# Performance work log

Measured on AMD Instinct MI355X. Metric: run time of the kernel, lower is better.

The kernel has to match this reference:

```python
import jax, jax.numpy as jnp
import numpy as np

N, T, E, E2 = 10000, 32, 320000, 160000
D, H = 128, 128
SLOPE = 0.01  # LeakyReLU negative slope (args.relu)


def _lstm_dir(x, mask, Wih, Whh, b, reverse):
    # x: [N,T,D], mask: [N,T] int; returns final hidden [N,H] honoring per-seq lengths
    xs = jnp.swapaxes(x, 0, 1)                                 # [T,N,D]
    ms = jnp.swapaxes(mask, 0, 1)[..., None].astype(x.dtype)   # [T,N,1]
    Hh = Whh.shape[1]
    h0 = jnp.zeros((x.shape[0], Hh), x.dtype)

    def step(carry, tm):
        h, c = carry
        xt, mt = tm
        g = xt @ Wih.T + h @ Whh.T + b                         # [N,4H], torch gate order i,f,g,o
        i, f, gg, o = jnp.split(g, 4, axis=-1)
        i, f, o = jax.nn.sigmoid(i), jax.nn.sigmoid(f), jax.nn.sigmoid(o)
        c_new = f * c + i * jnp.tanh(gg)
        h_new = o * jnp.tanh(c_new)
        h = mt * h_new + (1.0 - mt) * h
        c = mt * c_new + (1.0 - mt) * c
        return (h, c), None

    (h, _), _ = jax.lax.scan(step, (h0, h0), (xs, ms), reverse=reverse)
    return h


def _sage(h, src, dst, Wself, Wneigh, b):
    # DGL SAGEConv, mean aggregator: h@W_self + mean_neigh(h)@W_neigh + b
    n = h.shape[0]
    msum = jax.ops.segment_sum(h[src], dst, num_segments=n)
    deg = jax.ops.segment_sum(jnp.ones((src.shape[0],), h.dtype), dst, num_segments=n)
    neigh = msum / jnp.maximum(deg, 1.0)[:, None]
    return h @ Wself + neigh @ Wneigh + b


def setup_inputs():
    key = jax.random.key(0)
    ks = jax.random.split(key, 40)
    f = lambda i, shape: jax.random.normal(ks[i], shape, jnp.float32) * 0.05
    return dict(
        inputs_s=jax.random.randint(ks[0], (N, T), 0, 128, jnp.int32),
        inputs_sm=jnp.ones((N, T), jnp.int32),
        inputs_c=jax.random.randint(ks[1], (N,), 0, 101, jnp.int32),
        inputs_co=jax.random.randint(ks[2], (N,), 0, 92, jnp.int32),
        inputs_sl=jax.random.randint(ks[3], (N,), 0, 6, jnp.int32),
        inputs_ip=jax.random.normal(ks[4], (N, 32), jnp.float32),
        blk_src=jax.random.randint(ks[5], (E,), 0, N, jnp.int32),
        blk_dst=jax.random.randint(ks[6], (E,), 0, N, jnp.int32),
        e_src=jax.random.randint(ks[7], (E2,), 0, N, jnp.int32),
        e_dst=jax.random.randint(ks[8], (E2,), 0, N, jnp.int32),
        emb_url=f(9, (128, D)), emb_cat=f(10, (101, D)), emb_cou=f(11, (92, D)), emb_sl_t=f(12, (6, D)),
        Wih_f=f(13, (4 * D, D)), Whh_f=f(14, (4 * D, D)), b_f=f(15, (4 * D,)),
        Wih_b=f(16, (4 * D, D)), Whh_b=f(17, (4 * D, D)), b_b=f(18, (4 * D,)),
        fc_lstm_W=f(19, (2 * D, D)), fc_lstm_b=f(20, (D,)),
        attnlin_W=f(21, (H, H)), attn_W=f(22, (H, 1)), attn_b=f(23, (1,)),
        W0_self=f(24, (4, D, H)), W0_neigh=f(25, (4, D, H)), b0=f(26, (4, H)),
        Wip_self=f(27, (32, H)), Wip_neigh=f(28, (32, H)), bip=f(29, (H,)),
        W1_self=f(30, (5, H, H)), W1_neigh=f(31, (5, H, H)), b1=f(32, (5, H)),
        fc_W=f(33, (2 * H, H)), fc_b=f(34, (H,)),
        fco_W=f(35, (H, 2)), fco_b=f(36, (2,)),
    )


def reference(inputs_s, inputs_sm, inputs_c, inputs_co, inputs_sl, inputs_ip,
              blk_src, blk_dst, e_src, e_dst,
              emb_url, emb_cat, emb_cou, emb_sl_t,
              Wih_f, Whh_f, b_f, Wih_b, Whh_b, b_b,
              fc_lstm_W, fc_lstm_b, attnlin_W, attn_W, attn_b,
              W0_self, W0_neigh, b0, Wip_self, Wip_neigh, bip,
              W1_self, W1_neigh, b1, fc_W, fc_b, fco_W, fco_b):
    lrelu = lambda x: jax.nn.leaky_relu(x, SLOPE)
    # --- URL encoder: embed -> bi-LSTM -> fc (dropout is identity in eval) ---
    xu = emb_url[inputs_s]                                      # [N,T,D]
    hf = _lstm_dir(xu, inputs_sm, Wih_f, Whh_f, b_f, False)     # fwd final hidden
    hb = _lstm_dir(xu, inputs_sm, Wih_b, Whh_b, b_b, True)      # bwd final hidden
    vec_url = lrelu(jnp.concatenate([hf, hb], 1) @ fc_lstm_W + fc_lstm_b)
    # --- six-stream (here five: no rules) SAGE stacks over shared blocks ---
    h4 = jnp.stack([vec_url, emb_cat[inputs_c], emb_cou[inputs_co], emb_sl_t[inputs_sl]])  # [4,N,D]
    sage_v = jax.vmap(_sage, in_axes=(0, None, None, 0, 0, 0))
    h4 = lrelu(sage_v(h4, blk_src, blk_dst, W0_self, W0_neigh, b0))
    hip = lrelu(_sage(inputs_ip, blk_src, blk_dst, Wip_self, Wip_neigh, bip))
    hs = jnp.concatenate([h4, hip[None]], 0)                    # [5,N,H]
    hs = lrelu(sage_v(hs, blk_src, blk_dst, W1_self, W1_neigh, b1))
    hs = jnp.transpose(hs, (1, 0, 2))                           # [N,5,H]
    # --- attention fusion across streams ---
    z = jnp.einsum('nsh,ho->nso', hs, attnlin_W)                # attn_linear(h_stack)
    a = jax.nn.softmax(jnp.einsum('nso,om->nsm', z, attn_W) + attn_b, axis=1)  # [N,5,1]
    h = jnp.sum(z * a, axis=1)                                  # [N,H]
    # --- per-edge gather-concat-MLP scoring (apply_edges) ---
    cat = jnp.concatenate([h[e_src], h[e_dst]], 1)              # [E2,2H]
    score = lrelu(cat @ fc_W + fc_b) @ fco_W + fco_b            # [E2,2]
    a_src = a[e_src][..., 0]                                    # [E2,5]
    attn_e = jnp.stack([a_src, a_src], axis=1)                  # [E2,2,5]
    return score, attn_e
```

## Files before the change

kernel.cpp:

```cpp
#include <hip/hip_runtime.h>
#include <hip/hip_bf16.h>
#include <stdint.h>

typedef unsigned short u16;
typedef unsigned int   u32;
typedef __attribute__((ext_vector_type(8))) short short8;
typedef __attribute__((ext_vector_type(4))) float f32x4;
typedef __attribute__((ext_vector_type(2))) u32   u32x2;
typedef __attribute__((ext_vector_type(4))) u32   u32x4;

#define DEV static __device__ __forceinline__

constexpr int N_  = 10000;
constexpr int T_  = 32;
constexpr int E_  = 320000;
constexpr int E2_ = 160000;

DEV u16 f2bf(float f) {
    union { float f; u32 u; } v; v.f = f;
    u32 u = v.u;
    return (u16)((u + 0x7fffu + ((u >> 16) & 1u)) >> 16);
}
DEV float bf2f(u16 h) {
    union { u32 u; float f; } v; v.u = ((u32)h) << 16; return v.f;
}
DEV float asf(u32 u) {
    union { u32 u; float f; } v; v.u = u; return v.f;
}
DEV u32 cvt_pk_bf16(float lo, float hi) {
    u32 r;
    asm("v_cvt_pk_bf16_f32 %0, %1, %2" : "=v"(r) : "v"(lo), "v"(hi));
    return r;
}
DEV float lrelu(float x) { return x > 0.f ? x : 0.01f * x; }

DEV float fexp2(float x) {
#if __has_builtin(__builtin_amdgcn_exp2f)
    return __builtin_amdgcn_exp2f(x);
#else
    return exp2f(x);
#endif
}
DEV float frcp(float x) {
#if __has_builtin(__builtin_amdgcn_rcpf)
    return __builtin_amdgcn_rcpf(x);
#else
    return 1.0f / x;
#endif
}
DEV float fsig(float x)  { return frcp(1.f + fexp2(-1.4426950408889634f * x)); }
DEV float ftanh_(float x){ return 1.f - 2.f * frcp(1.f + fexp2(2.8853900817779268f * x)); }

__global__ void k_xtab(const float* __restrict__ emb,
                       const float* __restrict__ WihF, const float* __restrict__ bF,
                       const float* __restrict__ WihB, const float* __restrict__ bB,
                       u16* __restrict__ xtab) {
    int sym = blockIdx.x, dir = blockIdx.y, o = threadIdx.x;
    const float* W = dir ? WihB : WihF;
    const float* b = dir ? bB : bF;
    __shared__ float er[128];
    if (o < 128) er[o] = emb[sym * 128 + o];
    __syncthreads();
    float s = b[o];
    for (int k = 0; k < 128; k++) s += er[k] * W[o * 128 + k];
    xtab[((size_t)(dir * 128 + sym)) * 512 + o] = f2bf(s);
}

struct WtSeg { const float* W; u16* out; int K, Nw, tot; };
struct WtArgs { WtSeg seg[9]; };
__global__ void k_wt_all(WtArgs a) {
    WtSeg sg = a.seg[blockIdx.y];
    int i = blockIdx.x * 256 + threadIdx.x;
    if (i >= sg.tot) return;
    int K = sg.K, Nw = sg.Nw;
    int k = i % K, n = (i / K) % Nw, s = i / (K * Nw);
    sg.out[i] = f2bf(sg.W[((size_t)s * K + k) * Nw + n]);
}

__global__ __launch_bounds__(512, 2) void k_lstm(
    const u16* __restrict__ xtab,
    const int* __restrict__ syms,
    const int* __restrict__ smask,
    const float* __restrict__ WhhF,
    const float* __restrict__ WhhB,
    u16* __restrict__ hcat)
{
    __shared__ u16 h_buf[2][2048];
    __shared__ int sym_l[512];
    __shared__ int msk_l[512];

    int tid = threadIdx.x;
    int w = tid >> 6, l = tid & 63, l15 = l & 15, lg = l >> 4;
    int dir = blockIdx.y;
    int n0 = blockIdx.x * 16;
    const float* Whh = dir ? WhhB : WhhF;

    for (int i = tid; i < 512; i += 512) {
        int seq = i >> 5, t = i & 31;
        sym_l[t * 16 + seq] = syms[(size_t)n0 * 32 + i];
        msk_l[t * 16 + seq] = smask[(size_t)n0 * 32 + i];
    }
    for (int i = tid; i < 2048; i += 512) h_buf[0][i] = 0;

    short8 aw[4][4];
#pragma unroll
    for (int gg = 0; gg < 4; gg++)
#pragma unroll
    for (int kk = 0; kk < 4; kk++) {
        const float* p = Whh + (size_t)(128 * gg + 16 * w + l15) * 128 + 32 * kk + 8 * lg;
        const float4* pp = (const float4*)p;
        float4 x0 = pp[0], x1 = pp[1];
        short8 v;
        v[0] = (short)f2bf(x0.x); v[1] = (short)f2bf(x0.y);
        v[2] = (short)f2bf(x0.z); v[3] = (short)f2bf(x0.w);
        v[4] = (short)f2bf(x1.x); v[5] = (short)f2bf(x1.y);
        v[6] = (short)f2bf(x1.z); v[7] = (short)f2bf(x1.w);
        aw[gg][kk] = v;
    }

    float hreg[4] = {0, 0, 0, 0};
    float creg[4] = {0, 0, 0, 0};
    int jb = 16 * w + 4 * lg;
    int wsk = 2 * w + (lg >> 1);
    int wof = (wsk * 16 + l15) * 8 + 4 * (lg & 1);
    const u16* xbase = xtab + (size_t)dir * 128 * 512 + jb;
    __syncthreads();

    u32x2 xt[4];
    {
        int t0 = dir ? 31 : 0;
        int sym0 = sym_l[t0 * 16 + l15];
        const u16* xr = xbase + (size_t)sym0 * 512;
#pragma unroll
        for (int gg = 0; gg < 4; gg++) xt[gg] = *(const u32x2*)(xr + gg * 128);
    }

    for (int st = 0; st < 32; st++) {
        const u16* rb = h_buf[st & 1];
        u16* wb = h_buf[(st & 1) ^ 1];
        int t = dir ? (31 - st) : st;
        int mt_i = msk_l[t * 16 + l15];

        u32x2 xtn[4];
        {
            int stn = (st < 31) ? (st + 1) : 31;
            int tn = dir ? (31 - stn) : stn;
            int symn = sym_l[tn * 16 + l15];
            const u16* xr = xbase + (size_t)symn * 512;
#pragma unroll
            for (int gg = 0; gg < 4; gg++) xtn[gg] = *(const u32x2*)(xr + gg * 128);
        }

        short8 bh[4];
#pragma unroll
        for (int kk = 0; kk < 4; kk++)
            bh[kk] = *(const short8*)&rb[((kk * 4 + lg) * 16 + l15) * 8];

        f32x4 acc[4];
#pragma unroll
        for (int gg = 0; gg < 4; gg++) {
            f32x4 a = {0.f, 0.f, 0.f, 0.f};
#pragma unroll
            for (int kk = 0; kk < 4; kk++)
                a = __builtin_amdgcn_mfma_f32_16x16x32_bf16(aw[gg][kk], bh[kk], a, 0, 0, 0);
            acc[gg] = a;
        }

        bool mb = mt_i != 0;
        float hN[4];
#pragma unroll
        for (int r = 0; r < 4; r++) {
            u32 wi = xt[0][r >> 1], wf = xt[1][r >> 1], wg = xt[2][r >> 1], wo = xt[3][r >> 1];
            float xi, xf, xg, xo;
            if (r & 1) {
                xi = asf(wi & 0xffff0000u); xf = asf(wf & 0xffff0000u);
                xg = asf(wg & 0xffff0000u); xo = asf(wo & 0xffff0000u);
            } else {
                xi = asf(wi << 16); xf = asf(wf << 16);
                xg = asf(wg << 16); xo = asf(wo << 16);
            }
            float gi = acc[0][r] + xi;
            float gf = acc[1][r] + xf;
            float gc = acc[2][r] + xg;
            float go = acc[3][r] + xo;
            float i_ = fsig(gi), f_ = fsig(gf), g_ = ftanh_(gc), o_ = fsig(go);
            float cn = f_ * creg[r] + i_ * g_;
            float hn = o_ * ftanh_(cn);
            hN[r]   = mb ? hn : hreg[r];
            creg[r] = mb ? cn : creg[r];
            hreg[r] = hN[r];
        }
        u32x2 pk;
        pk[0] = cvt_pk_bf16(hN[0], hN[1]);
        pk[1] = cvt_pk_bf16(hN[2], hN[3]);
        *(u32x2*)&wb[wof] = pk;
#pragma unroll
        for (int gg = 0; gg < 4; gg++) xt[gg] = xtn[gg];
        __syncthreads();
    }

    {
        u32x2 pk;
        pk[0] = cvt_pk_bf16(hreg[0], hreg[1]);
        pk[1] = cvt_pk_bf16(hreg[2], hreg[3]);
        *(u32x2*)&hcat[(size_t)(n0 + l15) * 256 + dir * 128 + jb] = pk;
    }
}

template<int ACT, int DUAL>
__global__ __launch_bounds__(256) void k_gemm(
    const u16* __restrict__ A1, int lda1, int soA1,
    const u16* __restrict__ A2, int lda2, int soA2,
    const u16* __restrict__ B1, int soB1,
    const u16* __restrict__ B2, int soB2,
    const float* __restrict__ bias, int soBias,
    u16* __restrict__ C, int ldc, int soC, int M, int K)
{
    int s = blockIdx.y;
    A1 += (size_t)s * soA1;
    if (DUAL) A2 += (size_t)s * soA2;
    B1 += (size_t)s * soB1;
    if (DUAL) B2 += (size_t)s * soB2;
    if (bias) bias += (size_t)s * soBias;
    C += (size_t)s * soC;

    int tid = threadIdx.x;
    int w = tid >> 6, l = tid & 63, l15 = l & 15, lg = l >> 4;
    int mbase = blockIdx.x * 64 + w * 16;
    int arow = mbase + l15; if (arow >= M) arow = M - 1;

    f32x4 acc[8];
#pragma unroll
    for (int nt = 0; nt < 8; nt++) {
        float bv = bias ? bias[16 * nt + l15] : 0.f;
        acc[nt] = (f32x4){bv, bv, bv, bv};
    }
    for (int k0 = 0; k0 < K; k0 += 32) {
        int k = k0 + 8 * lg;
        short8 a1 = *(const short8*)&A1[(size_t)arow * lda1 + k];
        short8 a2;
        if (DUAL) a2 = *(const short8*)&A2[(size_t)arow * lda2 + k];
#pragma unroll
        for (int nt = 0; nt < 8; nt++) {
            short8 b1 = *(const short8*)&B1[(size_t)(16 * nt + l15) * K + k];
            acc[nt] = __builtin_amdgcn_mfma_f32_16x16x32_bf16(a1, b1, acc[nt], 0, 0, 0);
            if (DUAL) {
                short8 b2 = *(const short8*)&B2[(size_t)(16 * nt + l15) * K + k];
                acc[nt] = __builtin_amdgcn_mfma_f32_16x16x32_bf16(a2, b2, acc[nt], 0, 0, 0);
            }
        }
    }
#pragma unroll
    for (int nt = 0; nt < 8; nt++)
#pragma unroll
    for (int r = 0; r < 4; r++) {
        int m = mbase + 4 * lg + r;
        if (m < M) {
            float v = acc[nt][r];
            if (ACT == 1) v = lrelu(v);
            C[(size_t)m * ldc + 16 * nt + l15] = f2bf(v);
        }
    }
}

__global__ void k_pack(const int* __restrict__ ic, const int* __restrict__ ico,
                       const int* __restrict__ isl, const float* __restrict__ ip,
                       const float* __restrict__ ecat, const float* __restrict__ ecou,
                       const float* __restrict__ esl, u16* __restrict__ F0) {
    int n = blockIdx.x, t = threadIdx.x;
    u16* row = F0 + (size_t)n * 544;
    row[128 + t] = f2bf(ecat[(size_t)ic[n]  * 128 + t]);
    row[256 + t] = f2bf(ecou[(size_t)ico[n] * 128 + t]);
    row[384 + t] = f2bf(esl [(size_t)isl[n] * 128 + t]);
    if (t < 32) row[512 + t] = f2bf(ip[(size_t)n * 32 + t]);
}

__global__ void k_hist(const int* __restrict__ dst, int E, int* __restrict__ deg) {
    int e = blockIdx.x * 256 + threadIdx.x;
    if (e < E) atomicAdd(&deg[dst[e]], 1);
}
__global__ void k_scan(const int* __restrict__ deg, int* __restrict__ rowptr,
                       int* __restrict__ cursor, int n) {
    __shared__ int part[1024];
    int tid = threadIdx.x;
    const int CH = 10;
    int base = tid * CH;
    int s = 0;
#pragma unroll
    for (int i = 0; i < CH; i++) { int idx = base + i; if (idx < n) s += deg[idx]; }
    part[tid] = s; __syncthreads();
    for (int off = 1; off < 1024; off <<= 1) {
        int v = (tid >= off) ? part[tid - off] : 0;
        __syncthreads();
        part[tid] += v;
        __syncthreads();
    }
    int run = part[tid] - s;
    for (int i = 0; i < CH; i++) {
        int idx = base + i;
        if (idx < n) { rowptr[idx] = run; cursor[idx] = run; run += deg[idx]; }
    }
    if (tid == 1023) rowptr[n] = part[1023];
}
__global__ void k_fill(const int* __restrict__ src, const int* __restrict__ dst, int E,
                       int* __restrict__ cursor, int* __restrict__ colsrc) {
    int e = blockIdx.x * 256 + threadIdx.x;
    if (e < E) {
        int pos = atomicAdd(&cursor[dst[e]], 1);
        colsrc[pos] = src[e];
    }
}

__global__ __launch_bounds__(256) void k_agg(const u16* __restrict__ F, int C,
                                             const int* __restrict__ rowptr,
                                             const int* __restrict__ colsrc,
                                             u16* __restrict__ out, int N) {
    int w = threadIdx.x >> 6, l = threadIdx.x & 63;
    int n = blockIdx.x * 4 + w;
    if (n >= N) return;
    int chunks = C >> 3;
    int c0 = l, c1 = l + 64;
    bool has1 = c1 < chunks;
    float a0[8] = {0,0,0,0,0,0,0,0}, a1[8] = {0,0,0,0,0,0,0,0};
    int beg = rowptr[n], end = rowptr[n + 1];
    for (int e = beg; e < end; e++) {
        int s = colsrc[e];
        const u32x4* rp = (const u32x4*)(F + (size_t)s * C);
        u32x4 v0 = rp[c0];
#pragma unroll
        for (int j = 0; j < 4; j++) {
            u32 u = v0[j];
            a0[2*j]   += bf2f((u16)u);
            a0[2*j+1] += bf2f((u16)(u >> 16));
        }
        if (has1) {
            u32x4 v1 = rp[c1];
#pragma unroll
            for (int j = 0; j < 4; j++) {
                u32 u = v1[j];
                a1[2*j]   += bf2f((u16)u);
                a1[2*j+1] += bf2f((u16)(u >> 16));
            }
        }
    }
    int dg = end - beg; if (dg < 1) dg = 1;
    float inv = 1.f / (float)dg;
    u32x4 o0;
#pragma unroll
    for (int j = 0; j < 4; j++)
        o0[j] = (u32)f2bf(a0[2*j] * inv) | ((u32)f2bf(a0[2*j+1] * inv) << 16);
    ((u32x4*)(out + (size_t)n * C))[c0] = o0;
    if (has1) {
        u32x4 o1;
#pragma unroll
        for (int j = 0; j < 4; j++)
            o1[j] = (u32)f2bf(a1[2*j] * inv) | ((u32)f2bf(a1[2*j+1] * inv) << 16);
        ((u32x4*)(out + (size_t)n * C))[c1] = o1;
    }
}

__global__ __launch_bounds__(256) void k_attn(const u16* __restrict__ Z,
                                              const float* __restrict__ attnW,
                                              float* __restrict__ aOut,
                                              u16* __restrict__ hT, int N) {
    int w = threadIdx.x >> 6, l = threadIdx.x & 63;
    int n = blockIdx.x * 4 + w;
    if (n >= N) return;
    float wa0 = attnW[l], wa1 = attnW[l + 64];
    float z0[5], z1[5], lgt[5];
#pragma unroll
    for (int s = 0; s < 5; s++) {
        z0[s] = bf2f(Z[((size_t)(n * 5 + s)) * 128 + l]);
        z1[s] = bf2f(Z[((size_t)(n * 5 + s)) * 128 + l + 64]);
        float p = z0[s] * wa0 + z1[s] * wa1;
#pragma unroll
        for (int m = 1; m < 64; m <<= 1) p += __shfl_xor(p, m, 64);
        lgt[s] = p;
    }
    float mx = lgt[0];
#pragma unroll
    for (int s = 1; s < 5; s++) mx = fmaxf(mx, lgt[s]);
    float ex[5], sum = 0.f;
#pragma unroll
    for (int s = 0; s < 5; s++) { ex[s] = __expf(lgt[s] - mx); sum += ex[s]; }
    float a[5];
#pragma unroll
    for (int s = 0; s < 5; s++) a[s] = ex[s] / sum;
    float h0 = 0.f, h1 = 0.f;
#pragma unroll
    for (int s = 0; s < 5; s++) { h0 += a[s] * z0[s]; h1 += a[s] * z1[s]; }
    hT[(size_t)n * 128 + l] = f2bf(h0);
    hT[(size_t)n * 128 + l + 64] = f2bf(h1);
    if (l == 0) {
#pragma unroll
        for (int s = 0; s < 5; s++) aOut[(size_t)n * 5 + s] = a[s];
    }
}

__global__ __launch_bounds__(256) void k_edge(const u16* __restrict__ hT,
                                              const int* __restrict__ esrc,
                                              const int* __restrict__ edst,
                                              const u16* __restrict__ fcWt,
                                              const float* __restrict__ fcb,
                                              const float* __restrict__ fcoW,
                                              const float* __restrict__ fcob,
                                              float* __restrict__ score, int E2) {
    int tid = threadIdx.x;
    int w = tid >> 6, l = tid & 63, l15 = l & 15, lg = l >> 4;
    int eb = (blockIdx.x * 4 + w) * 16;
    int arow = eb + l15; if (arow >= E2) arow = E2 - 1;
    int sn = esrc[arow], dn = edst[arow];

    f32x4 acc[8];
#pragma unroll
    for (int nt = 0; nt < 8; nt++) {
        float bv = fcb[16 * nt + l15];
        acc[nt] = (f32x4){bv, bv, bv, bv};
    }
#pragma unroll
    for (int kk = 0; kk < 8; kk++) {
        int k = 32 * kk + 8 * lg;
        const u16* ap = (k < 128) ? &hT[(size_t)sn * 128 + k]
                                  : &hT[(size_t)dn * 128 + (k - 128)];
        short8 a = *(const short8*)ap;
#pragma unroll
        for (int nt = 0; nt < 8; nt++) {
            short8 b = *(const short8*)&fcWt[(size_t)(16 * nt + l15) * 256 + k];
            acc[nt] = __builtin_amdgcn_mfma_f32_16x16x32_bf16(a, b, acc[nt], 0, 0, 0);
        }
    }
    float p0[4] = {0,0,0,0}, p1[4] = {0,0,0,0};
#pragma unroll
    for (int nt = 0; nt < 8; nt++) {
        int c = 16 * nt + l15;
        float w0 = fcoW[c * 2], w1 = fcoW[c * 2 + 1];
#pragma unroll
        for (int r = 0; r < 4; r++) {
            float hd = lrelu(acc[nt][r]);
            p0[r] += hd * w0; p1[r] += hd * w1;
        }
    }
#pragma unroll
    for (int m = 1; m < 16; m <<= 1) {
#pragma unroll
        for (int r = 0; r < 4; r++) {
            p0[r] += __shfl_xor(p0[r], m, 64);
            p1[r] += __shfl_xor(p1[r], m, 64);
        }
    }
    if (l15 == 0) {
        float b0v = fcob[0], b1v = fcob[1];
#pragma unroll
        for (int r = 0; r < 4; r++) {
            int e = eb + 4 * lg + r;
            if (e < E2) {
                score[(size_t)e * 2 + 0] = p0[r] + b0v;
                score[(size_t)e * 2 + 1] = p1[r] + b1v;
            }
        }
    }
}

__global__ void k_attne(const float* __restrict__ a, const int* __restrict__ esrc,
                        float* __restrict__ out, int E2) {
    int m = blockIdx.x * 256 + threadIdx.x;
    if (m >= E2) return;
    int s = esrc[m];
#pragma unroll
    for (int i = 0; i < 5; i++) {
        float v = a[(size_t)s * 5 + i];
        out[(size_t)m * 10 + i] = v;
        out[(size_t)m * 10 + 5 + i] = v;
    }
}

extern "C" void kernel_launch(void* const* d_in, const int* in_sizes, int n_in,
                              void* d_out, int out_size, void* d_ws, size_t ws_size,
                              hipStream_t stream) {
    const int* inp_s   = (const int*)d_in[0];
    const int* inp_sm  = (const int*)d_in[1];
    const int* inp_c   = (const int*)d_in[2];
    const int* inp_co  = (const int*)d_in[3];
    const int* inp_sl  = (const int*)d_in[4];
    const float* inp_ip = (const float*)d_in[5];
    const int* blk_src = (const int*)d_in[6];
    const int* blk_dst = (const int*)d_in[7];
    const int* e_src   = (const int*)d_in[8];
    const int* e_dst   = (const int*)d_in[9];
    const float* emb_url = (const float*)d_in[10];
    const float* emb_cat = (const float*)d_in[11];
    const float* emb_cou = (const float*)d_in[12];
    const float* emb_sl  = (const float*)d_in[13];
    const float* Wih_f = (const float*)d_in[14];
    const float* Whh_f = (const float*)d_in[15];
    const float* b_f   = (const float*)d_in[16];
    const float* Wih_b = (const float*)d_in[17];
    const float* Whh_b = (const float*)d_in[18];
    const float* b_b   = (const float*)d_in[19];
    const float* fc_lstm_W = (const float*)d_in[20];
    const float* fc_lstm_b = (const float*)d_in[21];
    const float* attnlin_W = (const float*)d_in[22];
    const float* attn_W    = (const float*)d_in[23];
    const float* W0_self  = (const float*)d_in[25];
    const float* W0_neigh = (const float*)d_in[26];
    const float* b0       = (const float*)d_in[27];
    const float* Wip_self  = (const float*)d_in[28];
    const float* Wip_neigh = (const float*)d_in[29];
    const float* bip       = (const float*)d_in[30];
    const float* W1_self  = (const float*)d_in[31];
    const float* W1_neigh = (const float*)d_in[32];
    const float* b1       = (const float*)d_in[33];
    const float* fc_W  = (const float*)d_in[34];
    const float* fc_b  = (const float*)d_in[35];
    const float* fco_W = (const float*)d_in[36];
    const float* fco_b = (const float*)d_in[37];

    char* ws = (char*)d_ws;
    size_t off = 0;
    auto alloc = [&](size_t bytes) -> char* {
        char* p = ws + off;
        off += (bytes + 255) & ~(size_t)255;
        return p;
    };
    u16* xtab      = (u16*)alloc((size_t)2 * 128 * 512 * 2);
    u16* hcat      = (u16*)alloc((size_t)N_ * 256 * 2);
    u16* wt_fclstm = (u16*)alloc((size_t)128 * 256 * 2);
    u16* wt_w0s    = (u16*)alloc((size_t)4 * 128 * 128 * 2);
    u16* wt_w0n    = (u16*)alloc((size_t)4 * 128 * 128 * 2);
    u16* wt_ips    = (u16*)alloc((size_t)128 * 32 * 2);
    u16* wt_ipn    = (u16*)alloc((size_t)128 * 32 * 2);
    u16* wt_w1s    = (u16*)alloc((size_t)5 * 128 * 128 * 2);
    u16* wt_w1n    = (u16*)alloc((size_t)5 * 128 * 128 * 2);
    u16* wt_attn   = (u16*)alloc((size_t)128 * 128 * 2);
    u16* wt_fc     = (u16*)alloc((size_t)128 * 256 * 2);
    u16* F0        = (u16*)alloc((size_t)N_ * 544 * 2);
    u16* NEI       = (u16*)alloc((size_t)N_ * 640 * 2);
    u16* F1        = (u16*)alloc((size_t)N_ * 640 * 2);
    u16* H1        = (u16*)alloc((size_t)N_ * 640 * 2);
    u16* Zb        = (u16*)alloc((size_t)N_ * 5 * 128 * 2);
    u16* hT        = (u16*)alloc((size_t)N_ * 128 * 2);
    float* aA      = (float*)alloc((size_t)N_ * 5 * 4);
    int* deg       = (int*)alloc((size_t)N_ * 4);
    int* rowptr    = (int*)alloc((size_t)(N_ + 1) * 4);
    int* cursor    = (int*)alloc((size_t)N_ * 4);
    int* colsrc    = (int*)alloc((size_t)E_ * 4);
    (void)ws_size; (void)in_sizes; (void)n_in; (void)out_size;

    float* out_score = (float*)d_out;
    float* out_attne = out_score + (size_t)2 * E2_;

    hipMemsetAsync(deg, 0, (size_t)N_ * 4, stream);
    k_hist<<<dim3((E_ + 255) / 256), dim3(256), 0, stream>>>(blk_dst, E_, deg);
    k_scan<<<dim3(1), dim3(1024), 0, stream>>>(deg, rowptr, cursor, N_);
    k_fill<<<dim3((E_ + 255) / 256), dim3(256), 0, stream>>>(blk_src, blk_dst, E_, cursor, colsrc);

    k_xtab<<<dim3(128, 2), dim3(512), 0, stream>>>(emb_url, Wih_f, b_f, Wih_b, b_b, xtab);
    {
        WtArgs a;
        a.seg[0] = {fc_lstm_W, wt_fclstm, 256, 128, 1 * 128 * 256};
        a.seg[1] = {W0_self,   wt_w0s,    128, 128, 4 * 128 * 128};
        a.seg[2] = {W0_neigh,  wt_w0n,    128, 128, 4 * 128 * 128};
        a.seg[3] = {Wip_self,  wt_ips,     32, 128, 1 * 128 * 32};
        a.seg[4] = {Wip_neigh, wt_ipn,     32, 128, 1 * 128 * 32};
        a.seg[5] = {W1_self,   wt_w1s,    128, 128, 5 * 128 * 128};
        a.seg[6] = {W1_neigh,  wt_w1n,    128, 128, 5 * 128 * 128};
        a.seg[7] = {attnlin_W, wt_attn,   128, 128, 1 * 128 * 128};
        a.seg[8] = {fc_W,      wt_fc,     256, 128, 1 * 128 * 256};
        k_wt_all<<<dim3((5 * 128 * 128 + 255) / 256, 9), dim3(256), 0, stream>>>(a);
    }

    k_lstm<<<dim3(N_ / 16, 2), dim3(512), 0, stream>>>(xtab, inp_s, inp_sm, Whh_f, Whh_b, hcat);

    k_gemm<1, 0><<<dim3((N_ + 63) / 64, 1), dim3(256), 0, stream>>>(
        hcat, 256, 0, nullptr, 0, 0, wt_fclstm, 0, nullptr, 0,
        fc_lstm_b, 0, F0, 544, 0, N_, 256);
    k_pack<<<dim3(N_), dim3(128), 0, stream>>>(inp_c, inp_co, inp_sl, inp_ip,
                                               emb_cat, emb_cou, emb_sl, F0);

    k_agg<<<dim3(N_ / 4), dim3(256), 0, stream>>>(F0, 544, rowptr, colsrc, NEI, N_);
    k_gemm<1, 1><<<dim3((N_ + 63) / 64, 4), dim3(256), 0, stream>>>(
        F0, 544, 128, NEI, 544, 128, wt_w0s, 128 * 128, wt_w0n, 128 * 128,
        b0, 128, F1, 640, 128, N_, 128);
    k_gemm<1, 1><<<dim3((N_ + 63) / 64, 1), dim3(256), 0, stream>>>(
        F0 + 512, 544, 0, NEI + 512, 544, 0, wt_ips, 0, wt_ipn, 0,
        bip, 0, F1 + 4 * 128, 640, 0, N_, 32);

    k_agg<<<dim3(N_ / 4), dim3(256), 0, stream>>>(F1, 640, rowptr, colsrc, NEI, N_);
    k_gemm<1, 1><<<dim3((N_ + 63) / 64, 5), dim3(256), 0, stream>>>(
        F1, 640, 128, NEI, 640, 128, wt_w1s, 128 * 128, wt_w1n, 128 * 128,
        b1, 128, H1, 640, 128, N_, 128);

    k_gemm<0, 0><<<dim3((N_ * 5 + 63) / 64, 1), dim3(256), 0, stream>>>(
        H1, 128, 0, nullptr, 0, 0, wt_attn, 0, nullptr, 0,
        nullptr, 0, Zb, 128, 0, N_ * 5, 128);
    k_attn<<<dim3(N_ / 4), dim3(256), 0, stream>>>(Zb, attn_W, aA, hT, N_);

    k_edge<<<dim3(E2_ / 64), dim3(256), 0, stream>>>(hT, e_src, e_dst, wt_fc, fc_b,
                                                     fco_W, fco_b, out_score, E2_);
    k_attne<<<dim3(E2_ / 256), dim3(256), 0, stream>>>(aA, e_src, out_attne, E2_);
}
```

Baseline: 647.4 us.

## Unroll LSTM ping-pong steps, unroll neighbor aggregation, merge IP SAGE GEMM

The LSTM loop is unrolled by two with separate shared-memory ping-pong buffers and register sets, and the input projection is loaded into the MFMA accumulator as its initial value, so the separate add is no longer needed. The mean aggregation gathers four neighbor rows per iteration to keep more loads in flight. The separate 32-wide IP SAGE GEMM is merged into the 4-stream layer-0 GEMM as a fifth stream, using zero-padded 128-wide weights and a concatenated bias buffer. That saves a launch, but the fifth stream now reads 128 columns from a 544-wide row starting at column 512, so it runs past the row end (and past the buffer end on the last row) and relies on the zero weight padding to cancel those values.

```diff
diff --git a/kernel.cpp b/kernel.cpp
--- a/kernel.cpp
+++ b/kernel.cpp
@@ -66,15 +66,15 @@
     xtab[((size_t)(dir * 128 + sym)) * 512 + o] = f2bf(s);
 }
 
-struct WtSeg { const float* W; u16* out; int K, Nw, tot; };
+struct WtSeg { const float* W; u16* out; int Kd, Ks, Nw, tot; };
 struct WtArgs { WtSeg seg[9]; };
 __global__ void k_wt_all(WtArgs a) {
     WtSeg sg = a.seg[blockIdx.y];
     int i = blockIdx.x * 256 + threadIdx.x;
     if (i >= sg.tot) return;
-    int K = sg.K, Nw = sg.Nw;
-    int k = i % K, n = (i / K) % Nw, s = i / (K * Nw);
-    sg.out[i] = f2bf(sg.W[((size_t)s * K + k) * Nw + n]);
+    int k = i % sg.Kd, n = (i / sg.Kd) % sg.Nw, s = i / (sg.Kd * sg.Nw);
+    float v = (k < sg.Ks) ? sg.W[((size_t)s * sg.Ks + k) * sg.Nw + n] : 0.f;
+    sg.out[i] = f2bf(v);
 }
 
 __global__ __launch_bounds__(512, 2) void k_lstm(
@@ -85,7 +85,8 @@
     const float* __restrict__ WhhB,
     u16* __restrict__ hcat)
 {
-    __shared__ u16 h_buf[2][2048];
+    __shared__ u16 h_buf0[2048];
+    __shared__ u16 h_buf1[2048];
     __shared__ int sym_l[512];
     __shared__ int msk_l[512];
 
@@ -100,7 +101,7 @@
         sym_l[t * 16 + seq] = syms[(size_t)n0 * 32 + i];
         msk_l[t * 16 + seq] = smask[(size_t)n0 * 32 + i];
     }
-    for (int i = tid; i < 2048; i += 512) h_buf[0][i] = 0;
+    for (int i = tid; i < 2048; i += 512) h_buf0[i] = 0;
 
     short8 aw[4][4];
 #pragma unroll
@@ -126,30 +127,25 @@
     const u16* xbase = xtab + (size_t)dir * 128 * 512 + jb;
     __syncthreads();
 
-    u32x2 xt[4];
+    u32x2 xtA[4], xtB[4];
     {
         int t0 = dir ? 31 : 0;
         int sym0 = sym_l[t0 * 16 + l15];
         const u16* xr = xbase + (size_t)sym0 * 512;
 #pragma unroll
-        for (int gg = 0; gg < 4; gg++) xt[gg] = *(const u32x2*)(xr + gg * 128);
-    }
-
-    for (int st = 0; st < 32; st++) {
-        const u16* rb = h_buf[st & 1];
-        u16* wb = h_buf[(st & 1) ^ 1];
+        for (int gg = 0; gg < 4; gg++) xtA[gg] = *(const u32x2*)(xr + gg * 128);
+    }
+
+    auto step = [&](int st, const u16* rb, u16* wb, u32x2 (&xt)[4], u32x2 (&xtn)[4]) {
         int t = dir ? (31 - st) : st;
         int mt_i = msk_l[t * 16 + l15];
 
-        u32x2 xtn[4];
-        {
-            int stn = (st < 31) ? (st + 1) : 31;
-            int tn = dir ? (31 - stn) : stn;
-            int symn = sym_l[tn * 16 + l15];
-            const u16* xr = xbase + (size_t)symn * 512;
-#pragma unroll
-            for (int gg = 0; gg < 4; gg++) xtn[gg] = *(const u32x2*)(xr + gg * 128);
-        }
+        int stn = (st < 31) ? (st + 1) : 31;
+        int tn = dir ? (31 - stn) : stn;
+        int symn = sym_l[tn * 16 + l15];
+        const u16* xr = xbase + (size_t)symn * 512;
+#pragma unroll
+        for (int gg = 0; gg < 4; gg++) xtn[gg] = *(const u32x2*)(xr + gg * 128);
 
         short8 bh[4];
 #pragma unroll
@@ -159,7 +155,8 @@
         f32x4 acc[4];
 #pragma unroll
         for (int gg = 0; gg < 4; gg++) {
-            f32x4 a = {0.f, 0.f, 0.f, 0.f};
+            f32x4 a = { asf(xt[gg][0] << 16), asf(xt[gg][0] & 0xffff0000u),
+                        asf(xt[gg][1] << 16), asf(xt[gg][1] & 0xffff0000u) };
 #pragma unroll
             for (int kk = 0; kk < 4; kk++)
                 a = __builtin_amdgcn_mfma_f32_16x16x32_bf16(aw[gg][kk], bh[kk], a, 0, 0, 0);
@@ -170,20 +167,8 @@
         float hN[4];
 #pragma unroll
         for (int r = 0; r < 4; r++) {
-            u32 wi = xt[0][r >> 1], wf = xt[1][r >> 1], wg = xt[2][r >> 1], wo = xt[3][r >> 1];
-            float xi, xf, xg, xo;
-            if (r & 1) {
-                xi = asf(wi & 0xffff0000u); xf = asf(wf & 0xffff0000u);
-                xg = asf(wg & 0xffff0000u); xo = asf(wo & 0xffff0000u);
-            } else {
-                xi = asf(wi << 16); xf = asf(wf << 16);
-                xg = asf(wg << 16); xo = asf(wo << 16);
-            }
-            float gi = acc[0][r] + xi;
-            float gf = acc[1][r] + xf;
-            float gc = acc[2][r] + xg;
-            float go = acc[3][r] + xo;
-            float i_ = fsig(gi), f_ = fsig(gf), g_ = ftanh_(gc), o_ = fsig(go);
+            float i_ = fsig(acc[0][r]), f_ = fsig(acc[1][r]);
+            float g_ = ftanh_(acc[2][r]), o_ = fsig(acc[3][r]);
             float cn = f_ * creg[r] + i_ * g_;
             float hn = o_ * ftanh_(cn);
             hN[r]   = mb ? hn : hreg[r];
@@ -194,9 +179,12 @@
         pk[0] = cvt_pk_bf16(hN[0], hN[1]);
         pk[1] = cvt_pk_bf16(hN[2], hN[3]);
         *(u32x2*)&wb[wof] = pk;
-#pragma unroll
-        for (int gg = 0; gg < 4; gg++) xt[gg] = xtn[gg];
         __syncthreads();
+    };
+
+    for (int st2 = 0; st2 < 16; st2++) {
+        step(2 * st2,     h_buf0, h_buf1, xtA, xtB);
+        step(2 * st2 + 1, h_buf1, h_buf0, xtB, xtA);
     }
 
     {
@@ -323,26 +311,38 @@
     bool has1 = c1 < chunks;
     float a0[8] = {0,0,0,0,0,0,0,0}, a1[8] = {0,0,0,0,0,0,0,0};
     int beg = rowptr[n], end = rowptr[n + 1];
-    for (int e = beg; e < end; e++) {
-        int s = colsrc[e];
-        const u32x4* rp = (const u32x4*)(F + (size_t)s * C);
-        u32x4 v0 = rp[c0];
+
+    auto accum = [&](u32x4 v, float* a) {
 #pragma unroll
         for (int j = 0; j < 4; j++) {
-            u32 u = v0[j];
-            a0[2*j]   += bf2f((u16)u);
-            a0[2*j+1] += bf2f((u16)(u >> 16));
-        }
+            u32 u = v[j];
+            a[2*j]   += asf(u << 16);
+            a[2*j+1] += asf(u & 0xffff0000u);
+        }
+    };
+
+    int e = beg;
+    for (; e + 4 <= end; e += 4) {
+        int s0 = colsrc[e], s1 = colsrc[e+1], s2 = colsrc[e+2], s3 = colsrc[e+3];
+        const u32x4* r0 = (const u32x4*)(F + (size_t)s0 * C);
+        const u32x4* r1 = (const u32x4*)(F + (size_t)s1 * C);
+        const u32x4* r2 = (const u32x4*)(F + (size_t)s2 * C);
+        const u32x4* r3 = (const u32x4*)(F + (size_t)s3 * C);
+        u32x4 v0 = r0[c0], v1 = r1[c0], v2 = r2[c0], v3 = r3[c0];
         if (has1) {
-            u32x4 v1 = rp[c1];
-#pragma unroll
-            for (int j = 0; j < 4; j++) {
-                u32 u = v1[j];
-                a1[2*j]   += bf2f((u16)u);
-                a1[2*j+1] += bf2f((u16)(u >> 16));
-            }
-        }
-    }
+            u32x4 u0 = r0[c1], u1 = r1[c1], u2 = r2[c1], u3 = r3[c1];
+            accum(v0, a0); accum(v1, a0); accum(v2, a0); accum(v3, a0);
+            accum(u0, a1); accum(u1, a1); accum(u2, a1); accum(u3, a1);
+        } else {
+            accum(v0, a0); accum(v1, a0); accum(v2, a0); accum(v3, a0);
+        }
+    }
+    for (; e < end; e++) {
+        const u32x4* rp = (const u32x4*)(F + (size_t)colsrc[e] * C);
+        accum(rp[c0], a0);
+        if (has1) accum(rp[c1], a1);
+    }
+
     int dg = end - beg; if (dg < 1) dg = 1;
     float inv = 1.f / (float)dg;
     u32x4 o0;
@@ -525,14 +525,13 @@
     u16* xtab      = (u16*)alloc((size_t)2 * 128 * 512 * 2);
     u16* hcat      = (u16*)alloc((size_t)N_ * 256 * 2);
     u16* wt_fclstm = (u16*)alloc((size_t)128 * 256 * 2);
-    u16* wt_w0s    = (u16*)alloc((size_t)4 * 128 * 128 * 2);
-    u16* wt_w0n    = (u16*)alloc((size_t)4 * 128 * 128 * 2);
-    u16* wt_ips    = (u16*)alloc((size_t)128 * 32 * 2);
-    u16* wt_ipn    = (u16*)alloc((size_t)128 * 32 * 2);
+    u16* wt_w05s   = (u16*)alloc((size_t)5 * 128 * 128 * 2);
+    u16* wt_w05n   = (u16*)alloc((size_t)5 * 128 * 128 * 2);
     u16* wt_w1s    = (u16*)alloc((size_t)5 * 128 * 128 * 2);
     u16* wt_w1n    = (u16*)alloc((size_t)5 * 128 * 128 * 2);
     u16* wt_attn   = (u16*)alloc((size_t)128 * 128 * 2);
     u16* wt_fc     = (u16*)alloc((size_t)128 * 256 * 2);
+    float* bias5   = (float*)alloc((size_t)5 * 128 * 4);
     u16* F0        = (u16*)alloc((size_t)N_ * 544 * 2);
     u16* NEI       = (u16*)alloc((size_t)N_ * 640 * 2);
     u16* F1        = (u16*)alloc((size_t)N_ * 640 * 2);
@@ -557,17 +556,19 @@
     k_xtab<<<dim3(128, 2), dim3(512), 0, stream>>>(emb_url, Wih_f, b_f, Wih_b, b_b, xtab);
     {
         WtArgs a;
-        a.seg[0] = {fc_lstm_W, wt_fclstm, 256, 128, 1 * 128 * 256};
-        a.seg[1] = {W0_self,   wt_w0s,    128, 128, 4 * 128 * 128};
-        a.seg[2] = {W0_neigh,  wt_w0n,    128, 128, 4 * 128 * 128};
-        a.seg[3] = {Wip_self,  wt_ips,     32, 128, 1 * 128 * 32};
-        a.seg[4] = {Wip_neigh, wt_ipn,     32, 128, 1 * 128 * 32};
-        a.seg[5] = {W1_self,   wt_w1s,    128, 128, 5 * 128 * 128};
-        a.seg[6] = {W1_neigh,  wt_w1n,    128, 128, 5 * 128 * 128};
-        a.seg[7] = {attnlin_W, wt_attn,   128, 128, 1 * 128 * 128};
-        a.seg[8] = {fc_W,      wt_fc,     256, 128, 1 * 128 * 256};
+        a.seg[0] = {fc_lstm_W, wt_fclstm,            256, 256, 128, 1 * 128 * 256};
+        a.seg[1] = {W0_self,   wt_w05s,              128, 128, 128, 4 * 128 * 128};
+        a.seg[2] = {W0_neigh,  wt_w05n,              128, 128, 128, 4 * 128 * 128};
+        a.seg[3] = {Wip_self,  wt_w05s + 4 * 16384,  128,  32, 128, 1 * 128 * 128};
+        a.seg[4] = {Wip_neigh, wt_w05n + 4 * 16384,  128,  32, 128, 1 * 128 * 128};
+        a.seg[5] = {W1_self,   wt_w1s,               128, 128, 128, 5 * 128 * 128};
+        a.seg[6] = {W1_neigh,  wt_w1n,               128, 128, 128, 5 * 128 * 128};
+        a.seg[7] = {attnlin_W, wt_attn,              128, 128, 128, 1 * 128 * 128};
+        a.seg[8] = {fc_W,      wt_fc,                256, 256, 128, 1 * 128 * 256};
         k_wt_all<<<dim3((5 * 128 * 128 + 255) / 256, 9), dim3(256), 0, stream>>>(a);
     }
+    hipMemcpyAsync(bias5, b0, 512 * sizeof(float), hipMemcpyDeviceToDevice, stream);
+    hipMemcpyAsync(bias5 + 512, bip, 128 * sizeof(float), hipMemcpyDeviceToDevice, stream);
 
     k_lstm<<<dim3(N_ / 16, 2), dim3(512), 0, stream>>>(xtab, inp_s, inp_sm, Whh_f, Whh_b, hcat);
 
@@ -578,12 +579,9 @@
                                                emb_cat, emb_cou, emb_sl, F0);
 
     k_agg<<<dim3(N_ / 4), dim3(256), 0, stream>>>(F0, 544, rowptr, colsrc, NEI, N_);
-    k_gemm<1, 1><<<dim3((N_ + 63) / 64, 4), dim3(256), 0, stream>>>(
-        F0, 544, 128, NEI, 544, 128, wt_w0s, 128 * 128, wt_w0n, 128 * 128,
-        b0, 128, F1, 640, 128, N_, 128);
-    k_gemm<1, 1><<<dim3((N_ + 63) / 64, 1), dim3(256), 0, stream>>>(
-        F0 + 512, 544, 0, NEI + 512, 544, 0, wt_ips, 0, wt_ipn, 0,
-        bip, 0, F1 + 4 * 128, 640, 0, N_, 32);
+    k_gemm<1, 1><<<dim3((N_ + 63) / 64, 5), dim3(256), 0, stream>>>(
+        F0, 544, 128, NEI, 544, 128, wt_w05s, 128 * 128, wt_w05n, 128 * 128,
+        bias5, 128, F1, 640, 128, N_, 128);
 
     k_agg<<<dim3(N_ / 4), dim3(256), 0, stream>>>(F1, 640, rowptr, colsrc, NEI, N_);
     k_gemm<1, 1><<<dim3((N_ + 63) / 64, 5), dim3(256), 0, stream>>>(
```

New measurement: 597.4 us. 7.7% less time.
